# Performance work log

Measured on AMD Instinct MI355X. Metric: run time of the kernel, lower is better.

Reference implementation:

```python
import jax, jax.numpy as jnp
import numpy as np

N_HEADS = 16
D_EMBED = 1024


def setup_inputs() -> dict:
    key = jax.random.key(0)
    k_x, k_win, k_bin, k_wout, k_bout = jax.random.split(key, 5)
    B, S, D = 4, 2048, D_EMBED
    # weights stored as (in, out) so y = x @ W + b (equivalent to torch Linear)
    x = jax.random.normal(k_x, (B, S, D), dtype=jnp.float32)
    W_in = jax.random.normal(k_win, (D, 3 * D), dtype=jnp.float32) * (D ** -0.5)
    b_in = jax.random.normal(k_bin, (3 * D,), dtype=jnp.float32) * 0.02
    W_out = jax.random.normal(k_wout, (D, D), dtype=jnp.float32) * (D ** -0.5)
    b_out = jax.random.normal(k_bout, (D,), dtype=jnp.float32) * 0.02
    return {"x": x, "W_in": W_in, "b_in": b_in, "W_out": W_out, "b_out": b_out,
            "causal_mask": 1}


def reference(x, W_in, b_in, W_out, b_out, causal_mask):
    B, S, D = x.shape
    H = N_HEADS
    dh = D // H
    qkv = x @ W_in + b_in                      # [B,S,3D]
    q, k, v = jnp.split(qkv, 3, axis=-1)
    q = q.reshape(B, S, H, dh)
    k = k.reshape(B, S, H, dh)
    v = v.reshape(B, S, H, dh)
    scores = jnp.einsum('bqhd,bkhd->bhqk', q, k)   # [B,H,S,S]
    if causal_mask:
        # original masks with -inf BEFORE scaling; -inf/sqrt(dh) == -inf
        tri = jnp.triu(jnp.ones((S, S), dtype=bool), k=1)
        scores = jnp.where(tri, -jnp.inf, scores)
    scores = scores / jnp.sqrt(jnp.asarray(dh, dtype=scores.dtype))
    attn = jax.nn.softmax(scores, axis=-1)
    out = jnp.einsum('bhqk,bkhd->bqhd', attn, v).reshape(B, S, D)
    return out @ W_out + b_out
```

## Files before the change

kernel.cpp:

```cpp
#include <hip/hip_runtime.h>
#include <hip/hip_bf16.h>
#include <stdint.h>
#include <string.h>

#define S_LEN 2048
#define NH    16
#define DH    64
#define D_EMB 1024
#define CSCALE 0.18033688011112042f

typedef __attribute__((ext_vector_type(8)))  short short8;
typedef __attribute__((ext_vector_type(4)))  float f32x4;
typedef __attribute__((ext_vector_type(16))) float f32x16;
typedef __attribute__((ext_vector_type(4)))  uint32_t u32x4;

__device__ __forceinline__ unsigned short f2bf(float f) {
  uint32_t u = __builtin_bit_cast(uint32_t, f);
  uint32_t r = (u + 0x7FFFu + ((u >> 16) & 1u)) >> 16;
  return (unsigned short)r;
}

__device__ __forceinline__ uint32_t pkbf(float a, float b) {
  float2 f; f.x = a; f.y = b;
  __hip_bfloat162 h = __float22bfloat162_rn(f);
  uint32_t r;
  memcpy(&r, &h, 4);
  return r;
}

__device__ __forceinline__ uint32_t pktr(float a, float b) {
  return __builtin_amdgcn_perm(__builtin_bit_cast(uint32_t, b),
                               __builtin_bit_cast(uint32_t, a), 0x07060302u);
}

__device__ __forceinline__ float fexp2(float x) {
#if __has_builtin(__builtin_amdgcn_exp2f)
  return __builtin_amdgcn_exp2f(x);
#else
  float r;
  asm("v_exp_f32 %0, %1\ns_nop 0" : "=v"(r) : "v"(x));
  return r;
#endif
}

__device__ __forceinline__ void gload16(const void* g, void* l) {
  __builtin_amdgcn_global_load_lds(
      (__attribute__((address_space(1))) void*)(g),
      (__attribute__((address_space(3))) void*)(l),
      16, 0, 0);
}

__device__ __forceinline__ f32x16 mfma32(short8 a, short8 b, f32x16 c) {
  return __builtin_amdgcn_mfma_f32_32x32x16_bf16(a, b, c, 0, 0, 0);
}


__global__ __launch_bounds__(256)
void prep(const float* __restrict__ x, unsigned short* __restrict__ xb,
          const float* __restrict__ W_in, unsigned short* __restrict__ Wti,
          const float* __restrict__ W_out, unsigned short* __restrict__ Wto) {
  __shared__ float tsh[64][65];
  const int blk = blockIdx.x;
  const int tid = threadIdx.x;
  if (blk < 8192) {
    const int i = (blk * 256 + tid) * 4;
    float4 v = *(const float4*)&x[i];
    ushort4 o;
    o.x = f2bf(v.x); o.y = f2bf(v.y); o.z = f2bf(v.z); o.w = f2bf(v.w);
    *(ushort4*)&xb[i] = o;
    return;
  }
  const float* in; unsigned short* out; int C; int bid;
  if (blk < 8960) { in = W_in;  out = Wti; C = 3072; bid = blk - 8192; }
  else            { in = W_out; out = Wto; C = 1024; bid = blk - 8960; }
  const int br = (bid & 15) << 6;
  const int bc = (bid >> 4) << 6;
  const int tr = tid >> 4;
  const int tc = (tid & 15) << 2;
#pragma unroll
  for (int i = 0; i < 4; ++i) {
    float4 v = *(const float4*)&in[(size_t)(br + tr + i * 16) * C + bc + tc];
    tsh[tr + i * 16][tc + 0] = v.x;
    tsh[tr + i * 16][tc + 1] = v.y;
    tsh[tr + i * 16][tc + 2] = v.z;
    tsh[tr + i * 16][tc + 3] = v.w;
  }
  __syncthreads();
#pragma unroll
  for (int i = 0; i < 4; ++i) {
    int c = tr + i * 16;
    ushort4 o;
    o.x = f2bf(tsh[tc + 0][c]);
    o.y = f2bf(tsh[tc + 1][c]);
    o.z = f2bf(tsh[tc + 2][c]);
    o.w = f2bf(tsh[tc + 3][c]);
    *(ushort4*)&out[(size_t)(bc + c) * 1024 + br + tc] = o;
  }
}


template <int MODE>
__global__ __launch_bounds__(256, 3)
void gemm_bt(const unsigned short* __restrict__ A,
             const unsigned short* __restrict__ Bt,
             const float* __restrict__ bias,
             unsigned short* __restrict__ q_out,
             unsigned short* __restrict__ k_out,
             unsigned short* __restrict__ v_out,
             float* __restrict__ f_out,
             int M, int N, int K) {
  __shared__ __attribute__((aligned(16))) unsigned short As[128 * 64];
  __shared__ __attribute__((aligned(16))) unsigned short Bs[128 * 64];
  const int tid  = threadIdx.x;
  const int lane = tid & 63;
  const int w    = tid >> 6;
  const int grp  = lane >> 4;
  const int lc   = lane & 15;
  const int nbn  = N >> 7;
  const int bm   = blockIdx.x / nbn;
  const int bn   = blockIdx.x % nbn;
  const int wr   = w >> 1, wc = w & 1;

  f32x4 acc[4][4];
#pragma unroll
  for (int m = 0; m < 4; ++m)
#pragma unroll
    for (int n = 0; n < 4; ++n) acc[m][n] = f32x4{0.f, 0.f, 0.f, 0.f};

  const int srow = lane >> 3;
  const int scol = ((lane & 7) ^ srow) * 8;
  const int nkt  = K >> 6;

  for (int kt = 0; kt < nkt; ++kt) {
#pragma unroll
    for (int c = 0; c < 4; ++c) {
      const int rc = w * 32 + c * 8;
      gload16(&A[(size_t)(bm * 128 + rc + srow) * K + kt * 64 + scol],
              (void*)(&As[rc * 64]));
      gload16(&Bt[(size_t)(bn * 128 + rc + srow) * K + kt * 64 + scol],
              (void*)(&Bs[rc * 64]));
    }
    __syncthreads();
#pragma unroll
    for (int kk = 0; kk < 2; ++kk) {
      short8 af[4], bf[4];
#pragma unroll
      for (int m = 0; m < 4; ++m) {
        const int row = wr * 64 + m * 16 + lc;
        const int cb  = ((kk * 4 + grp) ^ (lc & 7)) * 8;
        af[m] = *(const short8*)(&As[row * 64 + cb]);
      }
#pragma unroll
      for (int n = 0; n < 4; ++n) {
        const int row = wc * 64 + n * 16 + lc;
        const int cb  = ((kk * 4 + grp) ^ (lc & 7)) * 8;
        bf[n] = *(const short8*)(&Bs[row * 64 + cb]);
      }
      __builtin_amdgcn_s_setprio(1);
#pragma unroll
      for (int m = 0; m < 4; ++m)
#pragma unroll
        for (int n = 0; n < 4; ++n)
          acc[m][n] = __builtin_amdgcn_mfma_f32_16x16x32_bf16(af[m], bf[n], acc[m][n], 0, 0, 0);
      __builtin_amdgcn_s_setprio(0);
    }
    __syncthreads();
  }

  const int gm0 = bm * 128 + wr * 64;
  const int gn0 = bn * 128 + wc * 64;
  if (MODE == 0) {
    const int seg = gn0 >> 10;
#pragma unroll
    for (int m = 0; m < 4; ++m) {
#pragma unroll
      for (int n = 0; n < 4; ++n) {
        const int gn = gn0 + n * 16 + lc;
        const float bv = bias[gn];
        const int j = gn & 1023;
        const int h = j >> 6, d = j & 63;
        const int gmb = gm0 + m * 16 + grp * 4;
        const int b = gmb >> 11;
        const size_t bhb = ((size_t)(b * NH + h) * 32 + ((gmb & 2047) >> 6)) * 4096;
        if (seg == 2) {
          const size_t vi = bhb + ((d >> 5) * 4 + m) * 512 +
                            ((d & 31) + (grp >> 1) * 32) * 8 + (grp & 1) * 4;
          uint2 dv;
          dv.x = pkbf(acc[m][n][0] + bv, acc[m][n][1] + bv);
          dv.y = pkbf(acc[m][n][2] + bv, acc[m][n][3] + bv);
          *(uint2*)&v_out[vi] = dv;
        } else {
#pragma unroll
          for (int r = 0; r < 4; ++r) {
            const int s = (gmb + r) & 2047;
            float v = acc[m][n][r] + bv;
            if (seg == 0) v *= CSCALE;
            const size_t idx = bhb + (((s >> 5) & 1) * 4 + (d >> 4)) * 512 +
                               ((s & 31) + ((d >> 3) & 1) * 32) * 8 + (d & 7);
            if (seg == 0) q_out[idx] = f2bf(v); else k_out[idx] = f2bf(v);
          }
        }
      }
    }
  } else {
#pragma unroll
    for (int m = 0; m < 4; ++m) {
#pragma unroll
      for (int n = 0; n < 4; ++n) {
        const int gn = gn0 + n * 16 + lc;
        const float bv = bias[gn];
#pragma unroll
        for (int r = 0; r < 4; ++r) {
          const int gm = gm0 + m * 16 + grp * 4 + r;
          f_out[(size_t)gm * N + gn] = acc[m][n][r] + bv;
        }
      }
    }
  }
}


__global__ __launch_bounds__(256, 4)
void attn_fwd11(const unsigned short* __restrict__ Qp,
                const unsigned short* __restrict__ Kp,
                const unsigned short* __restrict__ Vp,
                unsigned short* __restrict__ Aout) {
  __shared__ __attribute__((aligned(16))) unsigned short Ks[2][4096];
  __shared__ __attribute__((aligned(16))) unsigned short Vs[2][4096];
  const int tid  = threadIdx.x;
  const int lane = tid & 63, w = tid >> 6;
  const int q32  = lane & 31;
  const int hi   = lane >> 5;
  const int lof  = lane * 8;
  const int g    = blockIdx.x;
  const int t    = 15 - (g >> 6);
  const int bh   = (((g >> 3) & 7) << 3) | (g & 7);
  const int b    = bh >> 4, h = bh & 15;
  const size_t fb = (size_t)bh * 32;

#define STAGE(bf_, kb_) do {                                          \
    const size_t sb_ = (fb + (size_t)(kb_)) * 4096 + tid * 8;         \
    gload16(Kp + sb_,        (void*)&Ks[bf_][tid * 8]);               \
    gload16(Kp + sb_ + 2048, (void*)&Ks[bf_][2048 + tid * 8]);        \
    gload16(Vp + sb_,        (void*)&Vs[bf_][tid * 8]);               \
    gload16(Vp + sb_ + 2048, (void*)&Vs[bf_][2048 + tid * 8]);        \
  } while (0)

  const int qw0 = t * 128 + w * 32;
  const int qkb = 2 * t + (w >> 1), qsub = w & 1;

  short8 qf[4];
#pragma unroll
  for (int s = 0; s < 4; ++s)
    qf[s] = *(const short8*)(Qp + (fb + qkb) * 4096 + (qsub * 4 + s) * 512 + lof);

  f32x16 oa, ob;
#pragma unroll
  for (int rr = 0; rr < 16; ++rr) { oa[rr] = 0.f; ob[rr] = 0.f; }
  float l = 0.f;

  const int nbt = 2 * t + 2;
  STAGE(0, 0);

#pragma unroll 1
  for (int kb = 0; kb < nbt; ++kb) {
    const int cur = kb & 1;
    if (kb + 1 < nbt) {
      STAGE(cur ^ 1, kb + 1);
      asm volatile("s_waitcnt vmcnt(4)" ::: "memory");
    } else {
      asm volatile("s_waitcnt vmcnt(0)" ::: "memory");
    }
    __builtin_amdgcn_sched_barrier(0);
    __builtin_amdgcn_s_barrier();
    __builtin_amdgcn_sched_barrier(0);

    const int kvb = kb << 6;
    if (kvb <= qw0 + 31) {
      const unsigned short* kl = &Ks[cur][0];
      const unsigned short* vl = &Vs[cur][0];

      f32x16 c0, c1;
#pragma unroll
      for (int rr = 0; rr < 16; ++rr) { c0[rr] = 0.f; c1[rr] = -1e30f; }
      const bool do1 = (kvb + 32 <= qw0 + 31);
      __builtin_amdgcn_s_setprio(1);
#pragma unroll
      for (int s = 0; s < 4; ++s) {
        short8 kf = *(const short8*)(kl + s * 512 + lof);
        c0 = mfma32(kf, qf[s], c0);
      }
      if (do1) {
#pragma unroll
        for (int rr = 0; rr < 16; ++rr) c1[rr] = 0.f;
#pragma unroll
        for (int s = 0; s < 4; ++s) {
          short8 kf = *(const short8*)(kl + (4 + s) * 512 + lof);
          c1 = mfma32(kf, qf[s], c1);
        }
      }
      __builtin_amdgcn_s_setprio(0);

      if (kvb + 63 > qw0) {
        const int thr = qw0 + q32 - kvb;
#pragma unroll
        for (int rr = 0; rr < 16; ++rr) {
          const int k0 = (rr & 3) + 8 * (rr >> 2) + 4 * hi;
          if (k0 > thr)      c0[rr] = -1e30f;
          if (k0 + 32 > thr) c1[rr] = -1e30f;
        }
      }

#pragma unroll
      for (int rr = 0; rr < 16; ++rr) c0[rr] = fexp2(c0[rr]);
#pragma unroll
      for (int rr = 0; rr < 16; ++rr) c1[rr] = fexp2(c1[rr]);
      float tp[8];
#pragma unroll
      for (int i = 0; i < 8; ++i)
        tp[i] = (c0[i] + c0[i + 8]) + (c1[i] + c1[i + 8]);
      l += ((tp[0] + tp[1]) + (tp[2] + tp[3])) +
           ((tp[4] + tp[5]) + (tp[6] + tp[7]));

#pragma unroll
      for (int ks = 0; ks < 4; ++ks) {
        if (ks >= 2 && !do1) break;
        uint32_t pA, pB, pC, pD;
        if (ks == 0) {
          pA = pktr(c0[0],  c0[1]);  pB = pktr(c0[2],  c0[3]);
          pC = pktr(c0[4],  c0[5]);  pD = pktr(c0[6],  c0[7]);
        } else if (ks == 1) {
          pA = pktr(c0[8],  c0[9]);  pB = pktr(c0[10], c0[11]);
          pC = pktr(c0[12], c0[13]); pD = pktr(c0[14], c0[15]);
        } else if (ks == 2) {
          pA = pktr(c1[0],  c1[1]);  pB = pktr(c1[2],  c1[3]);
          pC = pktr(c1[4],  c1[5]);  pD = pktr(c1[6],  c1[7]);
        } else {
          pA = pktr(c1[8],  c1[9]);  pB = pktr(c1[10], c1[11]);
          pC = pktr(c1[12], c1[13]); pD = pktr(c1[14], c1[15]);
        }
        auto r0 = __builtin_amdgcn_permlane32_swap(pA, pC, false, false);
        auto r1 = __builtin_amdgcn_permlane32_swap(pB, pD, false, false);
        u32x4 fw; fw[0] = r0[0]; fw[1] = r1[0]; fw[2] = r0[1]; fw[3] = r1[1];
        const short8 frag = __builtin_bit_cast(short8, fw);
        oa = mfma32(*(const short8*)(vl + ks * 512 + lof), frag, oa);
        ob = mfma32(*(const short8*)(vl + (4 + ks) * 512 + lof), frag, ob);
      }
    }

    asm volatile("s_waitcnt lgkmcnt(0)" ::: "memory");
    __builtin_amdgcn_sched_barrier(0);
    __builtin_amdgcn_s_barrier();
    __builtin_amdgcn_sched_barrier(0);
  }

  l += __shfl_xor(l, 32);
  const float inv = 1.0f / l;
  unsigned short* ebuf = (unsigned short*)Ks;
  unsigned short* prow = ebuf + (w * 32 + q32) * 64;
  const int swz = (q32 & 7) << 3;
#pragma unroll
  for (int gg = 0; gg < 4; ++gg) {
    const int d0 = 8 * gg + 4 * hi;
    uint2 da, db;
    da.x = pkbf(oa[4 * gg] * inv,     oa[4 * gg + 1] * inv);
    da.y = pkbf(oa[4 * gg + 2] * inv, oa[4 * gg + 3] * inv);
    db.x = pkbf(ob[4 * gg] * inv,     ob[4 * gg + 1] * inv);
    db.y = pkbf(ob[4 * gg + 2] * inv, ob[4 * gg + 3] * inv);
    *(uint2*)&prow[d0 ^ swz]        = da;
    *(uint2*)&prow[(d0 + 32) ^ swz] = db;
  }
  asm volatile("s_waitcnt lgkmcnt(0)" ::: "memory");
  __builtin_amdgcn_sched_barrier(0);
  const int er = lane >> 1, eh = lane & 1;
  const int rswz = (er & 7) << 3;
  const unsigned short* lr = ebuf + (w * 32 + er) * 64;
  unsigned short* op = Aout + ((size_t)(b * S_LEN + qw0 + er)) * D_EMB + h * DH + eh * 32;
#pragma unroll
  for (int jj = 0; jj < 4; ++jj) {
    short8 ov = *(const short8*)&lr[(eh * 32 + jj * 8) ^ rswz];
    *(short8*)(op + jj * 8) = ov;
  }
#undef STAGE
}


extern "C" void kernel_launch(void* const* d_in, const int* in_sizes, int n_in,
                              void* d_out, int out_size, void* d_ws, size_t ws_size,
                              hipStream_t stream) {
  const float* x     = (const float*)d_in[0];
  const float* W_in  = (const float*)d_in[1];
  const float* b_in  = (const float*)d_in[2];
  const float* W_out = (const float*)d_in[3];
  const float* b_out = (const float*)d_in[4];

  char* ws = (char*)d_ws;
  unsigned short* xb  = (unsigned short*)(ws);
  unsigned short* Wti = (unsigned short*)(ws + 16777216);
  unsigned short* Wto = (unsigned short*)(ws + 23068672);
  unsigned short* Qb  = (unsigned short*)(ws + 25165824);
  unsigned short* Kb  = (unsigned short*)(ws + 41943040);
  unsigned short* Vb  = (unsigned short*)(ws + 58720256);
  float* out = (float*)d_out;

  prep<<<9216, 256, 0, stream>>>(x, xb, W_in, Wti, W_out, Wto);

  gemm_bt<0><<<64 * 24, 256, 0, stream>>>(xb, Wti, b_in, Qb, Kb, Vb, nullptr,
                                          8192, 3072, 1024);
  attn_fwd11<<<1024, 256, 0, stream>>>(Qb, Kb, Vb, xb);
  gemm_bt<1><<<64 * 8, 256, 0, stream>>>(xb, Wto, b_out, nullptr, nullptr, nullptr, out,
                                         8192, 1024, 1024);
}
```

Measured before the change: 151.4 us.

## Rewrite projection GEMMs as 8-wave 256x128 tiles with double-buffered LDS prefetch

Replaces the 4-wave 128x128 GEMM with an 8-wave, 512-thread kernel computing 256x128 tiles. It double-buffers the A and B tiles in LDS, issuing the next k-tile's global-to-LDS loads before computing the current one. The k-loop is split into four explicitly barriered MFMA phases with manual waitcnt and priority hints. The goal is to hide global load latency and raise reuse of each B tile. In exchange it uses more LDS (one block per CU), adds many block-wide barriers, and launches fewer, larger blocks.

```diff
diff --git a/kernel.cpp b/kernel.cpp
--- a/kernel.cpp
+++ b/kernel.cpp
@@ -52,6 +52,9 @@
 
 __device__ __forceinline__ f32x16 mfma32(short8 a, short8 b, f32x16 c) {
   return __builtin_amdgcn_mfma_f32_32x32x16_bf16(a, b, c, 0, 0, 0);
+}
+__device__ __forceinline__ f32x4 mfma16(short8 a, short8 b, f32x4 c) {
+  return __builtin_amdgcn_mfma_f32_16x16x32_bf16(a, b, c, 0, 0, 0);
 }
 
 
@@ -100,26 +103,27 @@
 
 
 template <int MODE>
-__global__ __launch_bounds__(256, 3)
-void gemm_bt(const unsigned short* __restrict__ A,
-             const unsigned short* __restrict__ Bt,
-             const float* __restrict__ bias,
-             unsigned short* __restrict__ q_out,
-             unsigned short* __restrict__ k_out,
-             unsigned short* __restrict__ v_out,
-             float* __restrict__ f_out,
-             int M, int N, int K) {
-  __shared__ __attribute__((aligned(16))) unsigned short As[128 * 64];
-  __shared__ __attribute__((aligned(16))) unsigned short Bs[128 * 64];
+__global__ __launch_bounds__(512, 1)
+void gemm8p(const unsigned short* __restrict__ A,
+            const unsigned short* __restrict__ Bt,
+            const float* __restrict__ bias,
+            unsigned short* __restrict__ q_out,
+            unsigned short* __restrict__ k_out,
+            unsigned short* __restrict__ v_out,
+            float* __restrict__ f_out,
+            int M, int N, int K) {
+  __shared__ __attribute__((aligned(16))) unsigned short As[2][256 * 64];
+  __shared__ __attribute__((aligned(16))) unsigned short Bs[2][128 * 64];
   const int tid  = threadIdx.x;
   const int lane = tid & 63;
-  const int w    = tid >> 6;
   const int grp  = lane >> 4;
   const int lc   = lane & 15;
+  const int w    = tid >> 6;
+  const int wr   = w >> 1, wc = w & 1;
   const int nbn  = N >> 7;
   const int bm   = blockIdx.x / nbn;
   const int bn   = blockIdx.x % nbn;
-  const int wr   = w >> 1, wc = w & 1;
+  const int nkt  = K >> 6;
 
   f32x4 acc[4][4];
 #pragma unroll
@@ -127,47 +131,115 @@
 #pragma unroll
     for (int n = 0; n < 4; ++n) acc[m][n] = f32x4{0.f, 0.f, 0.f, 0.f};
 
-  const int srow = lane >> 3;
-  const int scol = ((lane & 7) ^ srow) * 8;
-  const int nkt  = K >> 6;
+  const int sr8 = tid >> 3;
+  const int sc8 = tid & 7;
+  const int scs = ((sc8 ^ (sr8 & 7)) << 3);
+
+#define GS6(slot_, kt_) do {                                                  \
+    _Pragma("unroll")                                                         \
+    for (int c_ = 0; c_ < 4; ++c_)                                            \
+      gload16(&A[(size_t)(bm * 256 + c_ * 64 + sr8) * K + (kt_) * 64 + scs],  \
+              (void*)(&As[slot_][c_ * 4096 + tid * 8]));                      \
+    _Pragma("unroll")                                                         \
+    for (int c_ = 0; c_ < 2; ++c_)                                            \
+      gload16(&Bt[(size_t)(bn * 128 + c_ * 64 + sr8) * K + (kt_) * 64 + scs], \
+              (void*)(&Bs[slot_][c_ * 4096 + tid * 8]));                      \
+  } while (0)
+
+#define BARRIER() do {                          \
+    __builtin_amdgcn_sched_barrier(0);          \
+    __builtin_amdgcn_s_barrier();               \
+    __builtin_amdgcn_sched_barrier(0);          \
+  } while (0)
+#define LG0() do {                                              \
+    asm volatile("s_waitcnt lgkmcnt(0)" ::: "memory");          \
+    __builtin_amdgcn_sched_barrier(0);                          \
+  } while (0)
+
+  GS6(0, 0);
+  __syncthreads();
 
   for (int kt = 0; kt < nkt; ++kt) {
-#pragma unroll
-    for (int c = 0; c < 4; ++c) {
-      const int rc = w * 32 + c * 8;
-      gload16(&A[(size_t)(bm * 128 + rc + srow) * K + kt * 64 + scol],
-              (void*)(&As[rc * 64]));
-      gload16(&Bt[(size_t)(bn * 128 + rc + srow) * K + kt * 64 + scol],
-              (void*)(&Bs[rc * 64]));
-    }
-    __syncthreads();
-#pragma unroll
-    for (int kk = 0; kk < 2; ++kk) {
-      short8 af[4], bf[4];
-#pragma unroll
-      for (int m = 0; m < 4; ++m) {
-        const int row = wr * 64 + m * 16 + lc;
-        const int cb  = ((kk * 4 + grp) ^ (lc & 7)) * 8;
-        af[m] = *(const short8*)(&As[row * 64 + cb]);
-      }
-#pragma unroll
-      for (int n = 0; n < 4; ++n) {
-        const int row = wc * 64 + n * 16 + lc;
-        const int cb  = ((kk * 4 + grp) ^ (lc & 7)) * 8;
-        bf[n] = *(const short8*)(&Bs[row * 64 + cb]);
-      }
-      __builtin_amdgcn_s_setprio(1);
-#pragma unroll
-      for (int m = 0; m < 4; ++m)
-#pragma unroll
-        for (int n = 0; n < 4; ++n)
-          acc[m][n] = __builtin_amdgcn_mfma_f32_16x16x32_bf16(af[m], bf[n], acc[m][n], 0, 0, 0);
-      __builtin_amdgcn_s_setprio(0);
-    }
-    __syncthreads();
-  }
-
-  const int gm0 = bm * 128 + wr * 64;
+    const int slot = kt & 1;
+    const unsigned short* as = &As[slot][0];
+    const unsigned short* bs = &Bs[slot][0];
+    short8 af[4], bf[2];
+
+#pragma unroll
+    for (int m = 0; m < 4; ++m)
+      af[m] = *(const short8*)(as + (wr * 64 + m * 16 + lc) * 64 +
+                               ((grp ^ (lc & 7)) << 3));
+#pragma unroll
+    for (int n = 0; n < 2; ++n)
+      bf[n] = *(const short8*)(bs + (wc * 64 + n * 16 + lc) * 64 +
+                               ((grp ^ (lc & 7)) << 3));
+    if (kt + 1 < nkt) GS6(slot ^ 1, kt + 1);
+    BARRIER();
+    LG0();
+    __builtin_amdgcn_s_setprio(1);
+#pragma unroll
+    for (int m = 0; m < 4; ++m)
+#pragma unroll
+      for (int n = 0; n < 2; ++n)
+        acc[m][n] = mfma16(af[m], bf[n], acc[m][n]);
+    __builtin_amdgcn_s_setprio(0);
+    BARRIER();
+
+#pragma unroll
+    for (int n = 0; n < 2; ++n)
+      bf[n] = *(const short8*)(bs + (wc * 64 + (2 + n) * 16 + lc) * 64 +
+                               ((grp ^ (lc & 7)) << 3));
+    BARRIER();
+    LG0();
+    __builtin_amdgcn_s_setprio(1);
+#pragma unroll
+    for (int m = 0; m < 4; ++m)
+#pragma unroll
+      for (int n = 0; n < 2; ++n)
+        acc[m][2 + n] = mfma16(af[m], bf[n], acc[m][2 + n]);
+    __builtin_amdgcn_s_setprio(0);
+    BARRIER();
+
+#pragma unroll
+    for (int m = 0; m < 4; ++m)
+      af[m] = *(const short8*)(as + (wr * 64 + m * 16 + lc) * 64 +
+                               (((4 + grp) ^ (lc & 7)) << 3));
+#pragma unroll
+    for (int n = 0; n < 2; ++n)
+      bf[n] = *(const short8*)(bs + (wc * 64 + n * 16 + lc) * 64 +
+                               (((4 + grp) ^ (lc & 7)) << 3));
+    BARRIER();
+    LG0();
+    __builtin_amdgcn_s_setprio(1);
+#pragma unroll
+    for (int m = 0; m < 4; ++m)
+#pragma unroll
+      for (int n = 0; n < 2; ++n)
+        acc[m][n] = mfma16(af[m], bf[n], acc[m][n]);
+    __builtin_amdgcn_s_setprio(0);
+    BARRIER();
+
+#pragma unroll
+    for (int n = 0; n < 2; ++n)
+      bf[n] = *(const short8*)(bs + (wc * 64 + (2 + n) * 16 + lc) * 64 +
+                               (((4 + grp) ^ (lc & 7)) << 3));
+    asm volatile("s_waitcnt vmcnt(0)" ::: "memory");
+    BARRIER();
+    LG0();
+    __builtin_amdgcn_s_setprio(1);
+#pragma unroll
+    for (int m = 0; m < 4; ++m)
+#pragma unroll
+      for (int n = 0; n < 2; ++n)
+        acc[m][2 + n] = mfma16(af[m], bf[n], acc[m][2 + n]);
+    __builtin_amdgcn_s_setprio(0);
+    BARRIER();
+  }
+#undef GS6
+#undef BARRIER
+#undef LG0
+
+  const int gm0 = bm * 256 + wr * 64;
   const int gn0 = bn * 128 + wc * 64;
   if (MODE == 0) {
     const int seg = gn0 >> 10;
@@ -405,9 +477,9 @@
 
   prep<<<9216, 256, 0, stream>>>(x, xb, W_in, Wti, W_out, Wto);
 
-  gemm_bt<0><<<64 * 24, 256, 0, stream>>>(xb, Wti, b_in, Qb, Kb, Vb, nullptr,
-                                          8192, 3072, 1024);
+  gemm8p<0><<<768, 512, 0, stream>>>(xb, Wti, b_in, Qb, Kb, Vb, nullptr,
+                                     8192, 3072, 1024);
   attn_fwd11<<<1024, 256, 0, stream>>>(Qb, Kb, Vb, xb);
-  gemm_bt<1><<<64 * 8, 256, 0, stream>>>(xb, Wto, b_out, nullptr, nullptr, nullptr, out,
-                                         8192, 1024, 1024);
-}
+  gemm8p<1><<<256, 512, 0, stream>>>(xb, Wto, b_out, nullptr, nullptr, nullptr, out,
+                                     8192, 1024, 1024);
+}
```

Result: slower. 166.2 us (+9.8%).

## Load K/V fragments directly from global memory instead of LDS double buffering

Applied to the files above, without the earlier changes.

The attention kernel drops the shared-memory double-buffered K/V staging and its block-wide barriers. Each wave now reads its K and V MFMA fragments straight from global memory and loops only over its own causal range of key blocks, so waves no longer wait on each other. V fragments are prefetched into registers before the softmax. This removes LDS traffic and barrier stalls, but each wave re-reads K/V that other waves in the block also read, leaning on L2/L1 cache and adding global load latency with no explicit prefetch; launch bounds drop to 3 blocks per SIMD to allow more registers.

```diff
diff --git a/kernel.cpp b/kernel.cpp
--- a/kernel.cpp
+++ b/kernel.cpp
@@ -220,13 +220,12 @@
 }
 
 
-__global__ __launch_bounds__(256, 4)
-void attn_fwd11(const unsigned short* __restrict__ Qp,
+__global__ __launch_bounds__(256, 3)
+void attn_fwd12(const unsigned short* __restrict__ Qp,
                 const unsigned short* __restrict__ Kp,
                 const unsigned short* __restrict__ Vp,
                 unsigned short* __restrict__ Aout) {
-  __shared__ __attribute__((aligned(16))) unsigned short Ks[2][4096];
-  __shared__ __attribute__((aligned(16))) unsigned short Vs[2][4096];
+  __shared__ __attribute__((aligned(16))) unsigned short ebuf_s[4][32 * 64];
   const int tid  = threadIdx.x;
   const int lane = tid & 63, w = tid >> 6;
   const int q32  = lane & 31;
@@ -238,14 +237,6 @@
   const int b    = bh >> 4, h = bh & 15;
   const size_t fb = (size_t)bh * 32;
 
-#define STAGE(bf_, kb_) do {                                          \
-    const size_t sb_ = (fb + (size_t)(kb_)) * 4096 + tid * 8;         \
-    gload16(Kp + sb_,        (void*)&Ks[bf_][tid * 8]);               \
-    gload16(Kp + sb_ + 2048, (void*)&Ks[bf_][2048 + tid * 8]);        \
-    gload16(Vp + sb_,        (void*)&Vs[bf_][tid * 8]);               \
-    gload16(Vp + sb_ + 2048, (void*)&Vs[bf_][2048 + tid * 8]);        \
-  } while (0)
-
   const int qw0 = t * 128 + w * 32;
   const int qkb = 2 * t + (w >> 1), qsub = w & 1;
 
@@ -259,105 +250,97 @@
   for (int rr = 0; rr < 16; ++rr) { oa[rr] = 0.f; ob[rr] = 0.f; }
   float l = 0.f;
 
-  const int nbt = 2 * t + 2;
-  STAGE(0, 0);
+  const int nbtw = (qw0 >> 6) + 1;
 
 #pragma unroll 1
-  for (int kb = 0; kb < nbt; ++kb) {
-    const int cur = kb & 1;
-    if (kb + 1 < nbt) {
-      STAGE(cur ^ 1, kb + 1);
-      asm volatile("s_waitcnt vmcnt(4)" ::: "memory");
-    } else {
-      asm volatile("s_waitcnt vmcnt(0)" ::: "memory");
-    }
-    __builtin_amdgcn_sched_barrier(0);
-    __builtin_amdgcn_s_barrier();
-    __builtin_amdgcn_sched_barrier(0);
-
+  for (int kb = 0; kb < nbtw; ++kb) {
     const int kvb = kb << 6;
-    if (kvb <= qw0 + 31) {
-      const unsigned short* kl = &Ks[cur][0];
-      const unsigned short* vl = &Vs[cur][0];
-
-      f32x16 c0, c1;
-#pragma unroll
-      for (int rr = 0; rr < 16; ++rr) { c0[rr] = 0.f; c1[rr] = -1e30f; }
-      const bool do1 = (kvb + 32 <= qw0 + 31);
-      __builtin_amdgcn_s_setprio(1);
+    const bool do1 = (kvb + 32 <= qw0 + 31);
+    const unsigned short* kbase = Kp + (fb + (size_t)kb) * 4096;
+    const unsigned short* vbase = Vp + (fb + (size_t)kb) * 4096;
+
+    f32x16 c0, c1;
+#pragma unroll
+    for (int rr = 0; rr < 16; ++rr) { c0[rr] = 0.f; c1[rr] = -1e30f; }
+#pragma unroll
+    for (int s = 0; s < 4; ++s) {
+      short8 kf = *(const short8*)(kbase + s * 512 + lof);
+      c0 = mfma32(kf, qf[s], c0);
+    }
+    if (do1) {
+#pragma unroll
+      for (int rr = 0; rr < 16; ++rr) c1[rr] = 0.f;
 #pragma unroll
       for (int s = 0; s < 4; ++s) {
-        short8 kf = *(const short8*)(kl + s * 512 + lof);
-        c0 = mfma32(kf, qf[s], c0);
-      }
-      if (do1) {
-#pragma unroll
-        for (int rr = 0; rr < 16; ++rr) c1[rr] = 0.f;
-#pragma unroll
-        for (int s = 0; s < 4; ++s) {
-          short8 kf = *(const short8*)(kl + (4 + s) * 512 + lof);
-          c1 = mfma32(kf, qf[s], c1);
-        }
-      }
-      __builtin_amdgcn_s_setprio(0);
-
-      if (kvb + 63 > qw0) {
-        const int thr = qw0 + q32 - kvb;
-#pragma unroll
-        for (int rr = 0; rr < 16; ++rr) {
-          const int k0 = (rr & 3) + 8 * (rr >> 2) + 4 * hi;
-          if (k0 > thr)      c0[rr] = -1e30f;
-          if (k0 + 32 > thr) c1[rr] = -1e30f;
-        }
-      }
-
-#pragma unroll
-      for (int rr = 0; rr < 16; ++rr) c0[rr] = fexp2(c0[rr]);
-#pragma unroll
-      for (int rr = 0; rr < 16; ++rr) c1[rr] = fexp2(c1[rr]);
-      float tp[8];
-#pragma unroll
-      for (int i = 0; i < 8; ++i)
-        tp[i] = (c0[i] + c0[i + 8]) + (c1[i] + c1[i + 8]);
-      l += ((tp[0] + tp[1]) + (tp[2] + tp[3])) +
-           ((tp[4] + tp[5]) + (tp[6] + tp[7]));
-
-#pragma unroll
-      for (int ks = 0; ks < 4; ++ks) {
-        if (ks >= 2 && !do1) break;
-        uint32_t pA, pB, pC, pD;
-        if (ks == 0) {
-          pA = pktr(c0[0],  c0[1]);  pB = pktr(c0[2],  c0[3]);
-          pC = pktr(c0[4],  c0[5]);  pD = pktr(c0[6],  c0[7]);
-        } else if (ks == 1) {
-          pA = pktr(c0[8],  c0[9]);  pB = pktr(c0[10], c0[11]);
-          pC = pktr(c0[12], c0[13]); pD = pktr(c0[14], c0[15]);
-        } else if (ks == 2) {
-          pA = pktr(c1[0],  c1[1]);  pB = pktr(c1[2],  c1[3]);
-          pC = pktr(c1[4],  c1[5]);  pD = pktr(c1[6],  c1[7]);
-        } else {
-          pA = pktr(c1[8],  c1[9]);  pB = pktr(c1[10], c1[11]);
-          pC = pktr(c1[12], c1[13]); pD = pktr(c1[14], c1[15]);
-        }
-        auto r0 = __builtin_amdgcn_permlane32_swap(pA, pC, false, false);
-        auto r1 = __builtin_amdgcn_permlane32_swap(pB, pD, false, false);
-        u32x4 fw; fw[0] = r0[0]; fw[1] = r1[0]; fw[2] = r0[1]; fw[3] = r1[1];
-        const short8 frag = __builtin_bit_cast(short8, fw);
-        oa = mfma32(*(const short8*)(vl + ks * 512 + lof), frag, oa);
-        ob = mfma32(*(const short8*)(vl + (4 + ks) * 512 + lof), frag, ob);
-      }
-    }
-
-    asm volatile("s_waitcnt lgkmcnt(0)" ::: "memory");
-    __builtin_amdgcn_sched_barrier(0);
-    __builtin_amdgcn_s_barrier();
-    __builtin_amdgcn_sched_barrier(0);
+        short8 kf = *(const short8*)(kbase + (4 + s) * 512 + lof);
+        c1 = mfma32(kf, qf[s], c1);
+      }
+    }
+
+    short8 vf[8];
+#pragma unroll
+    for (int ks = 0; ks < 2; ++ks) {
+      vf[ks]     = *(const short8*)(vbase + ks * 512 + lof);
+      vf[4 + ks] = *(const short8*)(vbase + (4 + ks) * 512 + lof);
+    }
+    if (do1) {
+#pragma unroll
+      for (int ks = 2; ks < 4; ++ks) {
+        vf[ks]     = *(const short8*)(vbase + ks * 512 + lof);
+        vf[4 + ks] = *(const short8*)(vbase + (4 + ks) * 512 + lof);
+      }
+    }
+
+    if (kvb + 63 > qw0) {
+      const int thr = qw0 + q32 - kvb;
+#pragma unroll
+      for (int rr = 0; rr < 16; ++rr) {
+        const int k0 = (rr & 3) + 8 * (rr >> 2) + 4 * hi;
+        if (k0 > thr)      c0[rr] = -1e30f;
+        if (k0 + 32 > thr) c1[rr] = -1e30f;
+      }
+    }
+
+#pragma unroll
+    for (int rr = 0; rr < 16; ++rr) c0[rr] = fexp2(c0[rr]);
+#pragma unroll
+    for (int rr = 0; rr < 16; ++rr) c1[rr] = fexp2(c1[rr]);
+    float tp[8];
+#pragma unroll
+    for (int i = 0; i < 8; ++i)
+      tp[i] = (c0[i] + c0[i + 8]) + (c1[i] + c1[i + 8]);
+    l += ((tp[0] + tp[1]) + (tp[2] + tp[3])) +
+         ((tp[4] + tp[5]) + (tp[6] + tp[7]));
+
+#pragma unroll
+    for (int ks = 0; ks < 4; ++ks) {
+      if (ks >= 2 && !do1) break;
+      uint32_t pA, pB, pC, pD;
+      if (ks == 0) {
+        pA = pktr(c0[0],  c0[1]);  pB = pktr(c0[2],  c0[3]);
+        pC = pktr(c0[4],  c0[5]);  pD = pktr(c0[6],  c0[7]);
+      } else if (ks == 1) {
+        pA = pktr(c0[8],  c0[9]);  pB = pktr(c0[10], c0[11]);
+        pC = pktr(c0[12], c0[13]); pD = pktr(c0[14], c0[15]);
+      } else if (ks == 2) {
+        pA = pktr(c1[0],  c1[1]);  pB = pktr(c1[2],  c1[3]);
+        pC = pktr(c1[4],  c1[5]);  pD = pktr(c1[6],  c1[7]);
+      } else {
+        pA = pktr(c1[8],  c1[9]);  pB = pktr(c1[10], c1[11]);
+        pC = pktr(c1[12], c1[13]); pD = pktr(c1[14], c1[15]);
+      }
+      auto r0 = __builtin_amdgcn_permlane32_swap(pA, pC, false, false);
+      auto r1 = __builtin_amdgcn_permlane32_swap(pB, pD, false, false);
+      u32x4 fw; fw[0] = r0[0]; fw[1] = r1[0]; fw[2] = r0[1]; fw[3] = r1[1];
+      const short8 frag = __builtin_bit_cast(short8, fw);
+      oa = mfma32(vf[ks], frag, oa);
+      ob = mfma32(vf[4 + ks], frag, ob);
+    }
   }
 
   l += __shfl_xor(l, 32);
   const float inv = 1.0f / l;
-  unsigned short* ebuf = (unsigned short*)Ks;
-  unsigned short* prow = ebuf + (w * 32 + q32) * 64;
+  unsigned short* prow = &ebuf_s[w][q32 * 64];
   const int swz = (q32 & 7) << 3;
 #pragma unroll
   for (int gg = 0; gg < 4; ++gg) {
@@ -374,14 +357,13 @@
   __builtin_amdgcn_sched_barrier(0);
   const int er = lane >> 1, eh = lane & 1;
   const int rswz = (er & 7) << 3;
-  const unsigned short* lr = ebuf + (w * 32 + er) * 64;
+  const unsigned short* lr = &ebuf_s[w][er * 64];
   unsigned short* op = Aout + ((size_t)(b * S_LEN + qw0 + er)) * D_EMB + h * DH + eh * 32;
 #pragma unroll
   for (int jj = 0; jj < 4; ++jj) {
     short8 ov = *(const short8*)&lr[(eh * 32 + jj * 8) ^ rswz];
     *(short8*)(op + jj * 8) = ov;
   }
-#undef STAGE
 }
 
 
@@ -407,7 +389,7 @@
 
   gemm_bt<0><<<64 * 24, 256, 0, stream>>>(xb, Wti, b_in, Qb, Kb, Vb, nullptr,
                                           8192, 3072, 1024);
-  attn_fwd11<<<1024, 256, 0, stream>>>(Qb, Kb, Vb, xb);
+  attn_fwd12<<<1024, 256, 0, stream>>>(Qb, Kb, Vb, xb);
   gemm_bt<1><<<64 * 8, 256, 0, stream>>>(xb, Wto, b_out, nullptr, nullptr, nullptr, out,
                                          8192, 1024, 1024);
 }
```

Result: slower. 161.5 us (+6.7%).
